# Optimization experiments

Hardware: AMD Instinct MI355X
Metric: run time of the kernel (lower is better)

## Reference

```python
import jax, jax.numpy as jnp
import numpy as np

H = 128  # hidden_dim


def setup_inputs() -> dict:
    key = jax.random.key(0)
    k1, k2, k3 = jax.random.split(key, 3)
    N = 1024
    return {
        "node_emb": jax.random.normal(k1, (N, H), dtype=jnp.float32),
        "W1": jax.random.normal(k2, (2 * H, H), dtype=jnp.float32) * 0.05,
        "b1": jnp.zeros((H,), dtype=jnp.float32),
        "W2": jax.random.normal(k3, (H, 1), dtype=jnp.float32) * 0.05,
        "b2": jnp.zeros((1,), dtype=jnp.float32),
    }


def reference(node_emb, W1, b1, W2, b2):
    # L2 normalize rows (torch F.normalize: x / max(||x||, eps))
    norm = jnp.sqrt(jnp.sum(node_emb * node_emb, axis=-1, keepdims=True))
    e = node_emb / jnp.maximum(norm, 1e-12)  # (N, H)
    # adj[i, j] = mlp(cat(e_i, e_j)); split W1 so we never materialize (N,N,2H)
    left = e @ W1[:H]    # (N, H) contribution of e_i
    right = e @ W1[H:]   # (N, H) contribution of e_j
    h = jax.nn.relu(left[:, None, :] + right[None, :, :] + b1)  # (N, N, H)
    logits = jnp.einsum("ijh,h->ij", h, W2[:, 0]) + b2[0]       # (N, N)
    return jax.nn.softmax(logits, axis=-1)
```

## Files before the change

kernel.cpp:

```cpp
#include <hip/hip_runtime.h>

#define H 128
#define N 1024
#define SLOTS 144

__global__ __launch_bounds__(512) void prep_kernel(
    const float* __restrict__ x, const float* __restrict__ W1,
    const float* __restrict__ b1, const float* __restrict__ W2,
    float* __restrict__ LpS, float* __restrict__ Rt,
    float* __restrict__ c, int* __restrict__ meta)
{
    constexpr int PF = 8;
    __shared__ float e_s[4][H];
    __shared__ float cred[4][2];
    __shared__ int   slot_s[H];
    __shared__ int   cnt_s[2];
    __shared__ int   meta_s[3];
    const int t = threadIdx.x;
    const int i0 = blockIdx.x * 4;

    bool pos = false; int rank = 0;
    if (t < H) {
        const int lane = t & 63;
        pos = (W2[t] >= 0.f);
        const unsigned long long bal = __ballot(pos);
        rank = __popcll(bal & ((1ull << lane) - 1ull));
        if (lane == 0) cnt_s[t >> 6] = __popcll(bal);
    }
    if (t < 256) {
        const int row = t >> 6, lane = t & 63;
        const float2 v = *reinterpret_cast<const float2*>(&x[(i0 + row) * H + 2 * lane]);
        float s = v.x * v.x + v.y * v.y;
#pragma unroll
        for (int off = 32; off; off >>= 1) s += __shfl_xor(s, off);
        const float rn = 1.0f / fmaxf(sqrtf(s), 1e-12f);
        e_s[row][2 * lane]     = v.x * rn;
        e_s[row][2 * lane + 1] = v.y * rn;
    }
    __syncthreads();

    if (t < H) {
        const int c0 = cnt_s[0];
        const int P  = c0 + cnt_s[1];
        const int P8 = (P + 7) & ~7;
        const int lane = t & 63;
        int slot;
        if (pos) slot = (t < 64 ? 0 : c0) + rank;
        else     slot = P8 + (t < 64 ? 0 : 64 - c0) + (lane - rank);
        slot_s[t] = slot;
        if (t == 0) {
            meta_s[0] = P8;
            meta_s[1] = P8 + ((H - P + 7) & ~7);
            meta_s[2] = P;
        }
    }
    __syncthreads();

    const int h = t & (H - 1);
    const int q = t >> 7;
    const int r0 = (q & 1) * 2;
    const float* Wb = W1 + (q >= 2 ? H * H : 0) + h;

    float acc0 = 0.f, acc1 = 0.f;
    float wbuf[PF];
#pragma unroll
    for (int p = 0; p < PF; ++p) wbuf[p] = Wb[p * H];

    for (int kb = 0; kb < H - PF; kb += PF) {
#pragma unroll
        for (int p = 0; p < PF; ++p) {
            const float w = wbuf[p];
            wbuf[p] = Wb[(kb + p + PF) * H];
            acc0 = fmaf(e_s[r0][kb + p],     w, acc0);
            acc1 = fmaf(e_s[r0 + 1][kb + p], w, acc1);
        }
    }
#pragma unroll
    for (int p = 0; p < PF; ++p) {
        const int k = H - PF + p;
        acc0 = fmaf(e_s[r0][k],     wbuf[p], acc0);
        acc1 = fmaf(e_s[r0 + 1][k], wbuf[p], acc1);
    }

    const float w2h = W2[h];
    const int slot = slot_s[h];
    if (q < 2) {
        const float bb = b1[h];
        LpS[slot * N + (i0 + r0)]     = w2h * (acc0 + bb);
        LpS[slot * N + (i0 + r0 + 1)] = w2h * (acc1 + bb);
    } else {
        const float v0 = w2h * acc0, v1 = w2h * acc1;
        Rt[slot * N + (i0 + r0)]     = v0;
        Rt[slot * N + (i0 + r0 + 1)] = v1;
        float s0 = v0, s1 = v1;
#pragma unroll
        for (int off = 32; off; off >>= 1) {
            s0 += __shfl_xor(s0, off);
            s1 += __shfl_xor(s1, off);
        }
        const int wv = t >> 6;
        if ((t & 63) == 0) { cred[wv - 4][0] = s0; cred[wv - 4][1] = s1; }
    }
    __syncthreads();

    if (t < 4)
        c[i0 + t] = cred[(t >> 1) * 2][t & 1] + cred[(t >> 1) * 2 + 1][t & 1];

    {
        const int P8m = meta_s[0], T8m = meta_s[1], Pm = meta_s[2];
        const float4 z = {0.f, 0.f, 0.f, 0.f};
        if (t >= 64 && t < 72) {
            const int k = t - 64;
            if (k < P8m - Pm) {
                const int ps = Pm + k;
                *reinterpret_cast<float4*>(&LpS[ps * N + i0]) = z;
                *reinterpret_cast<float4*>(&Rt[ps * N + i0])  = z;
            }
        } else if (t >= 72 && t < 80) {
            const int k = t - 72;
            const int base2 = P8m + (H - Pm);
            if (k < T8m - base2) {
                const int ps = base2 + k;
                *reinterpret_cast<float4*>(&LpS[ps * N + i0]) = z;
                *reinterpret_cast<float4*>(&Rt[ps * N + i0])  = z;
            }
        }
    }
    if (blockIdx.x == 0 && t == 0) { meta[0] = meta_s[0]; meta[1] = meta_s[1]; }
}

__global__ __launch_bounds__(512) void adj_kernel(
    const float* __restrict__ LpS, const float* __restrict__ Rt,
    const float* __restrict__ c, const int* __restrict__ meta,
    float* __restrict__ out)
{
    constexpr int II = 4;
    __shared__ float4 LsT[SLOTS];
    __shared__ float red_m[II][8];
    __shared__ float red_s[II][8];

    const int t = threadIdx.x;
    const int lane = t & 63, wave = t >> 6;
    const int i0 = blockIdx.x * II;
    const int j0 = t * 2;

    const int P8 = meta[0], T8 = meta[1];

    if (t < T8)
        LsT[t] = *reinterpret_cast<const float4*>(&LpS[t * N + i0]);
    const float2 cj = *reinterpret_cast<const float2*>(&c[j0]);
    __syncthreads();

    float accx[II], accy[II];
#pragma unroll
    for (int ii = 0; ii < II; ++ii) { accx[ii] = cj.x; accy[ii] = cj.y; }

    const float* Rp = Rt + j0;
    float2 rbuf[8];
#pragma unroll
    for (int p = 0; p < 8; ++p)
        rbuf[p] = *reinterpret_cast<const float2*>(&Rp[p * N]);

    int hb = 0;
    for (; hb < P8; hb += 8) {
#pragma unroll
        for (int p = 0; p < 8; ++p) {
            const int s = hb + p;
            const float2 r = rbuf[p];
            rbuf[p] = *reinterpret_cast<const float2*>(&Rp[(s + 8) * N]);
            const float4 lv = LsT[s];
            const float* lp = &lv.x;
#pragma unroll
            for (int ii = 0; ii < II; ++ii) {
                accx[ii] += fabsf(lp[ii] + r.x);
                accy[ii] += fabsf(lp[ii] + r.y);
            }
        }
    }
    for (; hb < T8; hb += 8) {
#pragma unroll
        for (int p = 0; p < 8; ++p) {
            const int s = hb + p;
            const float2 r = rbuf[p];
            rbuf[p] = *reinterpret_cast<const float2*>(&Rp[(s + 8) * N]);
            const float4 lv = LsT[s];
            const float* lp = &lv.x;
#pragma unroll
            for (int ii = 0; ii < II; ++ii) {
                accx[ii] -= fabsf(lp[ii] + r.x);
                accy[ii] -= fabsf(lp[ii] + r.y);
            }
        }
    }

#pragma unroll
    for (int ii = 0; ii < II; ++ii) { accx[ii] *= 0.5f; accy[ii] *= 0.5f; }

#pragma unroll
    for (int ii = 0; ii < II; ++ii) {
        float m = fmaxf(accx[ii], accy[ii]);
#pragma unroll
        for (int off = 32; off; off >>= 1) m = fmaxf(m, __shfl_xor(m, off));
        if (lane == 0) red_m[ii][wave] = m;
    }
    __syncthreads();

    float mm[II];
#pragma unroll
    for (int ii = 0; ii < II; ++ii) {
        float m = red_m[ii][0];
#pragma unroll
        for (int w = 1; w < 8; ++w) m = fmaxf(m, red_m[ii][w]);
        mm[ii] = m;
    }

#pragma unroll
    for (int ii = 0; ii < II; ++ii) {
        accx[ii] = expf(accx[ii] - mm[ii]);
        accy[ii] = expf(accy[ii] - mm[ii]);
        float s = accx[ii] + accy[ii];
#pragma unroll
        for (int off = 32; off; off >>= 1) s += __shfl_xor(s, off);
        if (lane == 0) red_s[ii][wave] = s;
    }
    __syncthreads();

#pragma unroll
    for (int ii = 0; ii < II; ++ii) {
        float s = red_s[ii][0];
#pragma unroll
        for (int w = 1; w < 8; ++w) s += red_s[ii][w];
        const float r = 1.0f / s;
        float2 o;
        o.x = accx[ii] * r;
        o.y = accy[ii] * r;
        *reinterpret_cast<float2*>(&out[(i0 + ii) * N + j0]) = o;
    }
}

extern "C" void kernel_launch(void* const* d_in, const int* in_sizes, int n_in,
                              void* d_out, int out_size, void* d_ws, size_t ws_size,
                              hipStream_t stream) {
    const float* x  = (const float*)d_in[0];
    const float* W1 = (const float*)d_in[1];
    const float* b1 = (const float*)d_in[2];
    const float* W2 = (const float*)d_in[3];
    float* out = (float*)d_out;

    float* wsf = (float*)d_ws;
    float* LpS = wsf;
    float* Rt  = LpS + SLOTS * N;
    float* cc  = Rt + SLOTS * N;
    int*   meta = (int*)(cc + N);

    prep_kernel<<<N / 4, 512, 0, stream>>>(x, W1, b1, W2, LpS, Rt, cc, meta);
    adj_kernel<<<N / 4, 512, 0, stream>>>(LpS, Rt, cc, meta, out);
}
```

Before: 29.33 us.

## Stage prep outputs in LDS for float4 stores; use one column per adj thread

```diff
diff --git a/kernel.cpp b/kernel.cpp
--- a/kernel.cpp
+++ b/kernel.cpp
@@ -10,12 +10,14 @@
     float* __restrict__ LpS, float* __restrict__ Rt,
     float* __restrict__ c, int* __restrict__ meta)
 {
-    constexpr int PF = 8;
+    constexpr int PF = 16;
     __shared__ float e_s[4][H];
     __shared__ float cred[4][2];
     __shared__ int   slot_s[H];
     __shared__ int   cnt_s[2];
     __shared__ int   meta_s[3];
+    __shared__ float4 stageL[SLOTS];
+    __shared__ float4 stageR[SLOTS];
     const int t = threadIdx.x;
     const int i0 = blockIdx.x * 4;
 
@@ -84,14 +86,15 @@
 
     const float w2h = W2[h];
     const int slot = slot_s[h];
+    float* stg = q < 2 ? (float*)&stageL[slot] : (float*)&stageR[slot];
     if (q < 2) {
         const float bb = b1[h];
-        LpS[slot * N + (i0 + r0)]     = w2h * (acc0 + bb);
-        LpS[slot * N + (i0 + r0 + 1)] = w2h * (acc1 + bb);
+        stg[r0]     = w2h * (acc0 + bb);
+        stg[r0 + 1] = w2h * (acc1 + bb);
     } else {
         const float v0 = w2h * acc0, v1 = w2h * acc1;
-        Rt[slot * N + (i0 + r0)]     = v0;
-        Rt[slot * N + (i0 + r0 + 1)] = v1;
+        stg[r0]     = v0;
+        stg[r0 + 1] = v1;
         float s0 = v0, s1 = v1;
 #pragma unroll
         for (int off = 32; off; off >>= 1) {
@@ -101,104 +104,92 @@
         const int wv = t >> 6;
         if ((t & 63) == 0) { cred[wv - 4][0] = s0; cred[wv - 4][1] = s1; }
     }
-    __syncthreads();
-
-    if (t < 4)
-        c[i0 + t] = cred[(t >> 1) * 2][t & 1] + cred[(t >> 1) * 2 + 1][t & 1];
-
     {
         const int P8m = meta_s[0], T8m = meta_s[1], Pm = meta_s[2];
         const float4 z = {0.f, 0.f, 0.f, 0.f};
         if (t >= 64 && t < 72) {
             const int k = t - 64;
-            if (k < P8m - Pm) {
-                const int ps = Pm + k;
-                *reinterpret_cast<float4*>(&LpS[ps * N + i0]) = z;
-                *reinterpret_cast<float4*>(&Rt[ps * N + i0])  = z;
-            }
+            if (k < P8m - Pm) { stageL[Pm + k] = z; stageR[Pm + k] = z; }
         } else if (t >= 72 && t < 80) {
             const int k = t - 72;
             const int base2 = P8m + (H - Pm);
-            if (k < T8m - base2) {
-                const int ps = base2 + k;
-                *reinterpret_cast<float4*>(&LpS[ps * N + i0]) = z;
-                *reinterpret_cast<float4*>(&Rt[ps * N + i0])  = z;
-            }
-        }
-    }
+            if (k < T8m - base2) { stageL[base2 + k] = z; stageR[base2 + k] = z; }
+        }
+    }
+    __syncthreads();
+
+    const int T8 = meta_s[1];
+    if (t < 4)
+        c[i0 + t] = cred[(t >> 1) * 2][t & 1] + cred[(t >> 1) * 2 + 1][t & 1];
+    if (t < T8)
+        *reinterpret_cast<float4*>(&LpS[t * N + i0]) = stageL[t];
+    else if (t >= 256 && t < 256 + T8)
+        *reinterpret_cast<float4*>(&Rt[(t - 256) * N + i0]) = stageR[t - 256];
     if (blockIdx.x == 0 && t == 0) { meta[0] = meta_s[0]; meta[1] = meta_s[1]; }
 }
 
-__global__ __launch_bounds__(512) void adj_kernel(
+__global__ __launch_bounds__(1024) void adj_kernel(
     const float* __restrict__ LpS, const float* __restrict__ Rt,
     const float* __restrict__ c, const int* __restrict__ meta,
     float* __restrict__ out)
 {
     constexpr int II = 4;
     __shared__ float4 LsT[SLOTS];
-    __shared__ float red_m[II][8];
-    __shared__ float red_s[II][8];
+    __shared__ float red_m[II][16];
+    __shared__ float red_s[II][16];
 
     const int t = threadIdx.x;
     const int lane = t & 63, wave = t >> 6;
     const int i0 = blockIdx.x * II;
-    const int j0 = t * 2;
 
     const int P8 = meta[0], T8 = meta[1];
 
     if (t < T8)
         LsT[t] = *reinterpret_cast<const float4*>(&LpS[t * N + i0]);
-    const float2 cj = *reinterpret_cast<const float2*>(&c[j0]);
-    __syncthreads();
-
-    float accx[II], accy[II];
-#pragma unroll
-    for (int ii = 0; ii < II; ++ii) { accx[ii] = cj.x; accy[ii] = cj.y; }
-
-    const float* Rp = Rt + j0;
-    float2 rbuf[8];
-#pragma unroll
-    for (int p = 0; p < 8; ++p)
-        rbuf[p] = *reinterpret_cast<const float2*>(&Rp[p * N]);
+    const float cj = c[t];
+    __syncthreads();
+
+    float acc[II];
+#pragma unroll
+    for (int ii = 0; ii < II; ++ii) acc[ii] = cj;
+
+    const float* Rp = Rt + t;
+    float rbuf[8];
+#pragma unroll
+    for (int p = 0; p < 8; ++p) rbuf[p] = Rp[p * N];
 
     int hb = 0;
     for (; hb < P8; hb += 8) {
 #pragma unroll
         for (int p = 0; p < 8; ++p) {
             const int s = hb + p;
-            const float2 r = rbuf[p];
-            rbuf[p] = *reinterpret_cast<const float2*>(&Rp[(s + 8) * N]);
+            const float r = rbuf[p];
+            rbuf[p] = Rp[(s + 8) * N];
             const float4 lv = LsT[s];
             const float* lp = &lv.x;
 #pragma unroll
-            for (int ii = 0; ii < II; ++ii) {
-                accx[ii] += fabsf(lp[ii] + r.x);
-                accy[ii] += fabsf(lp[ii] + r.y);
-            }
+            for (int ii = 0; ii < II; ++ii) acc[ii] += fabsf(lp[ii] + r);
         }
     }
     for (; hb < T8; hb += 8) {
 #pragma unroll
         for (int p = 0; p < 8; ++p) {
             const int s = hb + p;
-            const float2 r = rbuf[p];
-            rbuf[p] = *reinterpret_cast<const float2*>(&Rp[(s + 8) * N]);
+            const float r = rbuf[p];
+            rbuf[p] = Rp[(s + 8) * N];
             const float4 lv = LsT[s];
             const float* lp = &lv.x;
 #pragma unroll
-            for (int ii = 0; ii < II; ++ii) {
-                accx[ii] -= fabsf(lp[ii] + r.x);
-                accy[ii] -= fabsf(lp[ii] + r.y);
-            }
-        }
-    }
-
-#pragma unroll
-    for (int ii = 0; ii < II; ++ii) { accx[ii] *= 0.5f; accy[ii] *= 0.5f; }
-
-#pragma unroll
-    for (int ii = 0; ii < II; ++ii) {
-        float m = fmaxf(accx[ii], accy[ii]);
+            for (int ii = 0; ii < II; ++ii) acc[ii] -= fabsf(lp[ii] + r);
+        }
+    }
+
+#pragma unroll
+    for (int ii = 0; ii < II; ++ii) acc[ii] *= 0.5f;
+
+#pragma unroll
+    for (int ii = 0; ii < II; ++ii) {
+        float m = acc[ii];
 #pragma unroll
         for (int off = 32; off; off >>= 1) m = fmaxf(m, __shfl_xor(m, off));
         if (lane == 0) red_m[ii][wave] = m;
@@ -210,15 +201,14 @@
     for (int ii = 0; ii < II; ++ii) {
         float m = red_m[ii][0];
 #pragma unroll
-        for (int w = 1; w < 8; ++w) m = fmaxf(m, red_m[ii][w]);
+        for (int w = 1; w < 16; ++w) m = fmaxf(m, red_m[ii][w]);
         mm[ii] = m;
     }
 
 #pragma unroll
     for (int ii = 0; ii < II; ++ii) {
-        accx[ii] = expf(accx[ii] - mm[ii]);
-        accy[ii] = expf(accy[ii] - mm[ii]);
-        float s = accx[ii] + accy[ii];
+        acc[ii] = expf(acc[ii] - mm[ii]);
+        float s = acc[ii];
 #pragma unroll
         for (int off = 32; off; off >>= 1) s += __shfl_xor(s, off);
         if (lane == 0) red_s[ii][wave] = s;
@@ -229,12 +219,8 @@
     for (int ii = 0; ii < II; ++ii) {
         float s = red_s[ii][0];
 #pragma unroll
-        for (int w = 1; w < 8; ++w) s += red_s[ii][w];
-        const float r = 1.0f / s;
-        float2 o;
-        o.x = accx[ii] * r;
-        o.y = accy[ii] * r;
-        *reinterpret_cast<float2*>(&out[(i0 + ii) * N + j0]) = o;
+        for (int w = 1; w < 16; ++w) s += red_s[ii][w];
+        out[(i0 + ii) * N + t] = acc[ii] * (1.0f / s);
     }
 }
 
@@ -254,5 +240,5 @@
     int*   meta = (int*)(cc + N);
 
     prep_kernel<<<N / 4, 512, 0, stream>>>(x, W1, b1, W2, LpS, Rt, cc, meta);
-    adj_kernel<<<N / 4, 512, 0, stream>>>(LpS, Rt, cc, meta, out);
+    adj_kernel<<<N / 4, 1024, 0, stream>>>(LpS, Rt, cc, meta, out);
 }
```

Result: slower. 30.22 us (+3.1%).
